# Kernel tuning notes

Hardware: AMD Instinct MI355X
Metric: run time of the kernel (lower is better)

Reference implementation:

```python
import jax, jax.numpy as jnp
import numpy as np

B, S, D = 2, 2048, 1024
H = 16
HD = D // H


def setup_inputs() -> dict:
    key = jax.random.key(0)
    k1, k2, k3 = jax.random.split(key, 3)
    x = jax.random.normal(k1, (B, S, D), dtype=jnp.float32)
    # nn.Linear(d, 3d, bias=False): weight [3d, d]; y = x @ W.T
    w_qkv = jax.random.normal(k2, (3 * D, D), dtype=jnp.float32) * (D ** -0.5)
    w_out = jax.random.normal(k3, (D, D), dtype=jnp.float32) * (D ** -0.5)
    return {"x": x, "w_qkv": w_qkv, "w_out": w_out}


def reference(x, w_qkv, w_out):
    batch, seq_len, _ = x.shape
    qkv = jnp.einsum('bsd,ed->bse', x, w_qkv)  # [B,S,3D]
    q, k, v = jnp.split(qkv, 3, axis=-1)
    # [B,S,D] -> [B,H,S,HD]
    def heads(t):
        return t.reshape(batch, seq_len, H, HD).transpose(0, 2, 1, 3)
    q, k, v = heads(q), heads(k), heads(v)
    scale = HD ** -0.5
    attn = jnp.einsum('bhqd,bhkd->bhqk', q, k) * scale  # [B,H,S,S]
    causal = jnp.triu(jnp.ones((seq_len, seq_len), dtype=bool), k=1)
    attn = jnp.where(causal, -jnp.inf, attn)
    attn = jax.nn.softmax(attn, axis=-1)
    out = jnp.einsum('bhqk,bhkd->bhqd', attn, v)  # [B,H,S,HD]
    out = out.transpose(0, 2, 1, 3).reshape(batch, seq_len, D)
    return jnp.einsum('bsd,ed->bse', out, w_out)
```

## Files before the change

kernel.cpp:

```cpp
#include <hip/hip_runtime.h>

#define NUM_B 2
#define SEQ   2048
#define DIM   1024
#define NH    16
#define HD    64

typedef __attribute__((ext_vector_type(8))) short short8;
typedef __attribute__((ext_vector_type(4))) float floatx4;
typedef unsigned short us;

#define QSCALE  0.18033688011112042f
#define SHIFT2  17.312340490667560f

#if __has_builtin(__builtin_amdgcn_exp2f)
#define EXP2(x) __builtin_amdgcn_exp2f(x)
#else
#define EXP2(x) exp2f(x)
#endif

__device__ __forceinline__ us f2bf(float f) {
    unsigned u = __float_as_uint(f);
    u += 0x7fffu + ((u >> 16) & 1u);
    return (us)(u >> 16);
}
__device__ __forceinline__ us f2bf_t(float f) {
    return (us)(__float_as_uint(f) >> 16);
}

#define GLD16(gptr, lptr) __builtin_amdgcn_global_load_lds( \
    (__attribute__((address_space(1))) unsigned int*)(gptr), \
    (__attribute__((address_space(3))) unsigned int*)(lptr), 16, 0, 0)

__global__ __launch_bounds__(256) void cast_all(
    const float* __restrict__ x, const float* __restrict__ wq,
    const float* __restrict__ wo, us* __restrict__ xb,
    us* __restrict__ wqb, us* __restrict__ wob)
{
    int i = blockIdx.x * 256 + threadIdx.x;
    const float* src; us* dst; int off;
    if (i < 524288)      { src = x;  dst = xb;  off = i; }
    else if (i < 917504) { src = wq; dst = wqb; off = i - 524288; }
    else                 { src = wo; dst = wob; off = i - 917504; }
    const float4* p = (const float4*)src + (size_t)off * 2;
    float4 f0 = p[0];
    float4 f1 = p[1];
    short8 v;
    v[0] = (short)f2bf(f0.x); v[1] = (short)f2bf(f0.y);
    v[2] = (short)f2bf(f0.z); v[3] = (short)f2bf(f0.w);
    v[4] = (short)f2bf(f1.x); v[5] = (short)f2bf(f1.y);
    v[6] = (short)f2bf(f1.z); v[7] = (short)f2bf(f1.w);
    *(short8*)(dst + (size_t)off * 8) = v;
}

__global__ __launch_bounds__(256, 2) void gemm_qkv(
    const us* __restrict__ A, const us* __restrict__ Bw,
    us* __restrict__ qb, us* __restrict__ kb, us* __restrict__ vt)
{
    __shared__ us As[128 * 64];
    __shared__ us Bs[128 * 64];
    const int t = threadIdx.x;
    const int lane = t & 63, w = t >> 6;
    const int l16 = lane & 15, quad = lane >> 4;
    const int wr = (w >> 1) * 64, wc = (w & 1) * 64;
    const int m0 = blockIdx.y * 128, n0 = blockIdx.x * 128;
    const bool isV = (blockIdx.x >= 16);
    const int srow = lane >> 3;
    const int soff = ((lane & 7) ^ srow) << 3;
    const int rsw  = l16 & 7;

    floatx4 acc[4][4];
    #pragma unroll
    for (int i = 0; i < 4; ++i)
        #pragma unroll
        for (int j = 0; j < 4; ++j) acc[i][j] = (floatx4){0.f, 0.f, 0.f, 0.f};

    for (int k0 = 0; k0 < DIM; k0 += 64) {
        #pragma unroll
        for (int c = 0; c < 4; ++c) {
            int chunk = w * 4 + c;
            int row = chunk * 8 + srow;
            GLD16(A  + (size_t)(m0 + row) * DIM + k0 + soff, &As[chunk * 512]);
            GLD16(Bw + (size_t)(n0 + row) * DIM + k0 + soff, &Bs[chunk * 512]);
        }
        __syncthreads();
        #pragma unroll
        for (int s = 0; s < 2; ++s) {
            short8 af[4], bf[4];
            #pragma unroll
            for (int i = 0; i < 4; ++i)
                af[i] = *(const short8*)&As[(wr + i * 16 + l16) * 64 + (((s * 4 + quad) ^ rsw) << 3)];
            #pragma unroll
            for (int j = 0; j < 4; ++j)
                bf[j] = *(const short8*)&Bs[(wc + j * 16 + l16) * 64 + (((s * 4 + quad) ^ rsw) << 3)];
            if (!isV) {
                #pragma unroll
                for (int i = 0; i < 4; ++i)
                    #pragma unroll
                    for (int j = 0; j < 4; ++j)
                        acc[i][j] = __builtin_amdgcn_mfma_f32_16x16x32_bf16(af[i], bf[j], acc[i][j], 0, 0, 0);
            } else {
                #pragma unroll
                for (int i = 0; i < 4; ++i)
                    #pragma unroll
                    for (int j = 0; j < 4; ++j)
                        acc[i][j] = __builtin_amdgcn_mfma_f32_16x16x32_bf16(bf[j], af[i], acc[i][j], 0, 0, 0);
            }
        }
        __syncthreads();
    }

    if (!isV) {
        const int which = n0 >> 10;
        const float sc = (which == 0) ? QSCALE : 1.0f;
        us* dst = (which == 0) ? qb : kb;
        #pragma unroll
        for (int i = 0; i < 4; ++i) {
            #pragma unroll
            for (int j = 0; j < 4; ++j) {
                int e = n0 + wc + j * 16 + l16;
                int h  = (e >> 6) & 15;
                int hd = e & 63;
                #pragma unroll
                for (int r = 0; r < 4; ++r) {
                    int m = m0 + wr + i * 16 + quad * 4 + r;
                    int b = m >> 11, s = m & 2047;
                    dst[((size_t)((b * NH + h) * SEQ + s) << 6) + hd] = f2bf(acc[i][j][r] * sc);
                }
            }
        }
    } else {
        #pragma unroll
        for (int i = 0; i < 4; ++i) {
            int m = m0 + wr + i * 16 + l16;
            int b = m >> 11, s = m & 2047;
            #pragma unroll
            for (int j = 0; j < 4; ++j) {
                int e0 = (n0 - 2048) + wc + j * 16 + quad * 4;
                #pragma unroll
                for (int r = 0; r < 4; ++r) {
                    int e = e0 + r;
                    int h = e >> 6, hd = e & 63;
                    vt[((size_t)((b * NH + h) * HD + hd) << 11) + s] = f2bf(acc[i][j][r]);
                }
            }
        }
    }
}

__global__ __launch_bounds__(256, 2) void gemm_out(
    const us* __restrict__ A, const us* __restrict__ Bw, float* __restrict__ outp)
{
    __shared__ us As[64 * 64];
    __shared__ us Bs[128 * 64];
    const int t = threadIdx.x;
    const int lane = t & 63, w = t >> 6;
    const int l16 = lane & 15, quad = lane >> 4;
    const int wr = (w >> 1) * 32, wc = (w & 1) * 64;
    const int m0 = blockIdx.y * 64, n0 = blockIdx.x * 128;
    const int srow = lane >> 3;
    const int soff = ((lane & 7) ^ srow) << 3;
    const int rsw  = l16 & 7;

    floatx4 acc[2][4];
    #pragma unroll
    for (int i = 0; i < 2; ++i)
        #pragma unroll
        for (int j = 0; j < 4; ++j) acc[i][j] = (floatx4){0.f, 0.f, 0.f, 0.f};

    for (int k0 = 0; k0 < DIM; k0 += 64) {
        #pragma unroll
        for (int c = 0; c < 2; ++c) {
            int chunk = w * 2 + c;
            int row = chunk * 8 + srow;
            GLD16(A + (size_t)(m0 + row) * DIM + k0 + soff, &As[chunk * 512]);
        }
        #pragma unroll
        for (int c = 0; c < 4; ++c) {
            int chunk = w * 4 + c;
            int row = chunk * 8 + srow;
            GLD16(Bw + (size_t)(n0 + row) * DIM + k0 + soff, &Bs[chunk * 512]);
        }
        __syncthreads();
        #pragma unroll
        for (int s = 0; s < 2; ++s) {
            short8 af[2], bf[4];
            #pragma unroll
            for (int i = 0; i < 2; ++i)
                af[i] = *(const short8*)&As[(wr + i * 16 + l16) * 64 + (((s * 4 + quad) ^ rsw) << 3)];
            #pragma unroll
            for (int j = 0; j < 4; ++j)
                bf[j] = *(const short8*)&Bs[(wc + j * 16 + l16) * 64 + (((s * 4 + quad) ^ rsw) << 3)];
            #pragma unroll
            for (int i = 0; i < 2; ++i)
                #pragma unroll
                for (int j = 0; j < 4; ++j)
                    acc[i][j] = __builtin_amdgcn_mfma_f32_16x16x32_bf16(af[i], bf[j], acc[i][j], 0, 0, 0);
        }
        __syncthreads();
    }

    #pragma unroll
    for (int i = 0; i < 2; ++i)
        #pragma unroll
        for (int j = 0; j < 4; ++j) {
            int n = n0 + wc + j * 16 + l16;
            #pragma unroll
            for (int r = 0; r < 4; ++r) {
                int m = m0 + wr + i * 16 + quad * 4 + r;
                outp[(size_t)m * DIM + n] = acc[i][j][r];
            }
        }
}

__global__ __launch_bounds__(128, 3) void attn(
    const us* __restrict__ qb, const us* __restrict__ kb,
    const us* __restrict__ vt, us* __restrict__ ob)
{
    __shared__ us Ks[64 * 64];
    __shared__ us Vs[64 * 64];
    __shared__ us Ps[2 * 32 * 72];
    const int t = threadIdx.x;
    const int lane = t & 63, w = t >> 6;
    const int l16 = lane & 15, quad = lane >> 4;
    const int idx = blockIdx.x;
    const int qt = 31 - (idx >> 5);
    const int bh = idx & 31;
    const int b = bh >> 4, h = bh & 15;
    const int q0 = qt << 6;
    const int wrow = q0 + w * 32;
    const size_t base = (size_t)bh * SEQ * HD;
    const us* qbh = qb + base;
    const us* kbh = kb + base;
    const us* vth = vt + base;
    us* Pp = Ps + w * 32 * 72;
    const int srow = lane >> 3;
    const int soff = ((lane & 7) ^ srow) << 3;
    const int rsw  = l16 & 7;

    short8 qa[2][2];
    #pragma unroll
    for (int g = 0; g < 2; ++g)
        #pragma unroll
        for (int s = 0; s < 2; ++s)
            qa[g][s] = *(const short8*)(qbh + (size_t)(wrow + g * 16 + l16) * HD + s * 32 + quad * 8);

    floatx4 o[2][4];
    #pragma unroll
    for (int g = 0; g < 2; ++g)
        #pragma unroll
        for (int j = 0; j < 4; ++j) o[g][j] = (floatx4){0.f, 0.f, 0.f, 0.f};
    float lrow[2][4] = {};

    for (int kt = 0; kt <= qt; ++kt) {
        const int j0 = kt << 6;
        #pragma unroll
        for (int c = 0; c < 4; ++c) {
            int chunk = w * 4 + c;
            int row = chunk * 8 + srow;
            GLD16(kbh + (size_t)(j0 + row) * HD + soff, &Ks[chunk * 512]);
            GLD16(vth + (size_t)row * SEQ + j0 + soff, &Vs[chunk * 512]);
        }
        __syncthreads();

        floatx4 sf[2][4];
        #pragma unroll
        for (int g = 0; g < 2; ++g)
            #pragma unroll
            for (int j = 0; j < 4; ++j)
                sf[g][j] = (floatx4){-SHIFT2, -SHIFT2, -SHIFT2, -SHIFT2};
        #pragma unroll
        for (int s = 0; s < 2; ++s)
            #pragma unroll
            for (int j = 0; j < 4; ++j) {
                short8 kf = *(const short8*)&Ks[(j * 16 + l16) * 64 + (((s * 4 + quad) ^ rsw) << 3)];
                #pragma unroll
                for (int g = 0; g < 2; ++g)
                    sf[g][j] = __builtin_amdgcn_mfma_f32_16x16x32_bf16(qa[g][s], kf, sf[g][j], 0, 0, 0);
            }

        if (kt == qt) {
            #pragma unroll
            for (int g = 0; g < 2; ++g) {
                int rowb = wrow + g * 16 + quad * 4;
                #pragma unroll
                for (int j = 0; j < 4; ++j) {
                    int colg = j0 + j * 16 + l16;
                    #pragma unroll
                    for (int r = 0; r < 4; ++r)
                        if (colg > rowb + r) sf[g][j][r] = -1e30f;
                }
            }
        }

        #pragma unroll
        for (int g = 0; g < 2; ++g) {
            float p[4][4];
            #pragma unroll
            for (int j = 0; j < 4; ++j)
                #pragma unroll
                for (int r = 0; r < 4; ++r) {
                    p[j][r] = EXP2(sf[g][j][r]);
                    Pp[(g * 16 + quad * 4 + r) * 72 + j * 16 + l16] = f2bf_t(p[j][r]);
                }
            #pragma unroll
            for (int r = 0; r < 4; ++r)
                lrow[g][r] += (p[0][r] + p[1][r]) + (p[2][r] + p[3][r]);
        }

        short8 pf[2][2];
        #pragma unroll
        for (int g = 0; g < 2; ++g)
            #pragma unroll
            for (int s = 0; s < 2; ++s)
                pf[g][s] = *(const short8*)&Pp[(g * 16 + l16) * 72 + s * 32 + quad * 8];
        #pragma unroll
        for (int s = 0; s < 2; ++s)
            #pragma unroll
            for (int j = 0; j < 4; ++j) {
                short8 vf = *(const short8*)&Vs[(j * 16 + l16) * 64 + (((s * 4 + quad) ^ rsw) << 3)];
                #pragma unroll
                for (int g = 0; g < 2; ++g)
                    o[g][j] = __builtin_amdgcn_mfma_f32_16x16x32_bf16(pf[g][s], vf, o[g][j], 0, 0, 0);
            }
        __syncthreads();
    }

    #pragma unroll
    for (int g = 0; g < 2; ++g)
        #pragma unroll
        for (int r = 0; r < 4; ++r) {
            float l = lrow[g][r];
            l += __shfl_xor(l, 1);
            l += __shfl_xor(l, 2);
            l += __shfl_xor(l, 4);
            l += __shfl_xor(l, 8);
            float inv = 1.0f / l;
            int grow = wrow + g * 16 + quad * 4 + r;
            #pragma unroll
            for (int j = 0; j < 4; ++j) {
                float val = o[g][j][r] * inv;
                ob[(size_t)(b * SEQ + grow) * DIM + h * HD + j * 16 + l16] = f2bf(val);
            }
        }
}

extern "C" void kernel_launch(void* const* d_in, const int* in_sizes, int n_in,
                              void* d_out, int out_size, void* d_ws, size_t ws_size,
                              hipStream_t stream) {
    const float* x     = (const float*)d_in[0];
    const float* w_qkv = (const float*)d_in[1];
    const float* w_out = (const float*)d_in[2];
    float* out = (float*)d_out;
    us* ws = (us*)d_ws;

    const size_t M1 = (size_t)1024 * 1024;
    us* xb  = ws;
    us* wqb = xb  + 4 * M1;
    us* wob = wqb + 3 * M1;
    us* qb  = wob + 1 * M1;
    us* kb  = qb  + 4 * M1;
    us* vt  = kb  + 4 * M1;
    us* obf = vt  + 4 * M1;

    cast_all<<<4096, 256, 0, stream>>>(x, w_qkv, w_out, xb, wqb, wob);
    gemm_qkv<<<dim3(24, 32), 256, 0, stream>>>(xb, wqb, qb, kb, vt);
    attn<<<1024, 128, 0, stream>>>(qb, kb, vt, obf);
    gemm_out<<<dim3(8, 64), 256, 0, stream>>>(obf, wob, out);
}
```

Baseline: 176.3 us.

## Rewrite attention with single-wave 32x32 MFMA tiles and register-shuffled P

The attention kernel now runs one 64-lane wave per block over 32 query rows and uses 32x32x16 MFMA with a transposed S = K·Q^T. P is passed to the PV MFMA through packed bf16 cross-half lane shuffles instead of a shared-memory round trip. K/V tiles are loaded into registers and the next tile's global-to-LDS load is issued before compute, overlapping memory with math. The grid doubles to 2048 blocks. In exchange, the 32-row causal tiles waste work on the diagonal 64-key tile, and register pressure rises with launch bounds of (64,2).

```diff
diff --git a/kernel.cpp b/kernel.cpp
--- a/kernel.cpp
+++ b/kernel.cpp
@@ -8,6 +8,8 @@
 
 typedef __attribute__((ext_vector_type(8))) short short8;
 typedef __attribute__((ext_vector_type(4))) float floatx4;
+typedef __attribute__((ext_vector_type(16))) float floatx16;
+typedef __attribute__((ext_vector_type(4))) unsigned int uint4v;
 typedef unsigned short us;
 
 #define QSCALE  0.18033688011112042f
@@ -24,8 +26,8 @@
     u += 0x7fffu + ((u >> 16) & 1u);
     return (us)(u >> 16);
 }
-__device__ __forceinline__ us f2bf_t(float f) {
-    return (us)(__float_as_uint(f) >> 16);
+__device__ __forceinline__ unsigned pk2(float lo, float hi) {
+    return (__float_as_uint(lo) >> 16) | (__float_as_uint(hi) & 0xFFFF0000u);
 }
 
 #define GLD16(gptr, lptr) __builtin_amdgcn_global_load_lds( \
@@ -213,136 +215,143 @@
         }
 }
 
-__global__ __launch_bounds__(128, 3) void attn(
+__global__ __launch_bounds__(64, 2) void attn(
     const us* __restrict__ qb, const us* __restrict__ kb,
     const us* __restrict__ vt, us* __restrict__ ob)
 {
     __shared__ us Ks[64 * 64];
     __shared__ us Vs[64 * 64];
-    __shared__ us Ps[2 * 32 * 72];
-    const int t = threadIdx.x;
-    const int lane = t & 63, w = t >> 6;
-    const int l16 = lane & 15, quad = lane >> 4;
+    const int lane = threadIdx.x;
+    const int l31 = lane & 31, hi = lane >> 5;
     const int idx = blockIdx.x;
-    const int qt = 31 - (idx >> 5);
+    const int qi = 63 - (idx >> 5);
     const int bh = idx & 31;
     const int b = bh >> 4, h = bh & 15;
-    const int q0 = qt << 6;
-    const int wrow = q0 + w * 32;
+    const int q0 = qi << 5;
+    const int nk = (qi >> 1) + 1;
     const size_t base = (size_t)bh * SEQ * HD;
     const us* qbh = qb + base;
     const us* kbh = kb + base;
     const us* vth = vt + base;
-    us* Pp = Ps + w * 32 * 72;
     const int srow = lane >> 3;
     const int soff = ((lane & 7) ^ srow) << 3;
-    const int rsw  = l16 & 7;
-
-    short8 qa[2][2];
-    #pragma unroll
-    for (int g = 0; g < 2; ++g)
-        #pragma unroll
-        for (int s = 0; s < 2; ++s)
-            qa[g][s] = *(const short8*)(qbh + (size_t)(wrow + g * 16 + l16) * HD + s * 32 + quad * 8);
-
-    floatx4 o[2][4];
-    #pragma unroll
-    for (int g = 0; g < 2; ++g)
-        #pragma unroll
-        for (int j = 0; j < 4; ++j) o[g][j] = (floatx4){0.f, 0.f, 0.f, 0.f};
-    float lrow[2][4] = {};
-
-    for (int kt = 0; kt <= qt; ++kt) {
-        const int j0 = kt << 6;
+    const int x7 = l31 & 7;
+
+    short8 qa[4];
+    #pragma unroll
+    for (int s = 0; s < 4; ++s)
+        qa[s] = *(const short8*)(qbh + (size_t)(q0 + l31) * HD + s * 16 + hi * 8);
+
+    floatx16 o[2];
+    #pragma unroll
+    for (int db = 0; db < 2; ++db)
+        #pragma unroll
+        for (int e = 0; e < 16; ++e) o[db][e] = 0.f;
+    float lsum = 0.f;
+
+    #pragma unroll
+    for (int ch = 0; ch < 8; ++ch) {
+        int row = ch * 8 + srow;
+        GLD16(kbh + (size_t)row * HD + soff, &Ks[ch * 512]);
+        GLD16(vth + (size_t)row * SEQ + soff, &Vs[ch * 512]);
+    }
+
+    for (int kt = 0; kt < nk; ++kt) {
+        __syncthreads();
+
+        short8 kf[2][4], vf[2][4];
+        #pragma unroll
+        for (int kb2 = 0; kb2 < 2; ++kb2)
+            #pragma unroll
+            for (int s = 0; s < 4; ++s)
+                kf[kb2][s] = *(const short8*)&Ks[(kb2 * 32 + l31) * 64 + (((2 * s + hi) ^ x7) << 3)];
+        #pragma unroll
+        for (int db = 0; db < 2; ++db)
+            #pragma unroll
+            for (int c = 0; c < 4; ++c)
+                vf[db][c] = *(const short8*)&Vs[(db * 32 + l31) * 64 + (((2 * c + hi) ^ x7) << 3)];
+
+        __syncthreads();
+
+        if (kt + 1 < nk) {
+            const int j0n = (kt + 1) << 6;
+            #pragma unroll
+            for (int ch = 0; ch < 8; ++ch) {
+                int row = ch * 8 + srow;
+                GLD16(kbh + (size_t)(j0n + row) * HD + soff, &Ks[ch * 512]);
+                GLD16(vth + (size_t)row * SEQ + j0n + soff, &Vs[ch * 512]);
+            }
+        }
+
+        floatx16 st[2];
+        #pragma unroll
+        for (int kb2 = 0; kb2 < 2; ++kb2)
+            #pragma unroll
+            for (int e = 0; e < 16; ++e) st[kb2][e] = -SHIFT2;
+        #pragma unroll
+        for (int kb2 = 0; kb2 < 2; ++kb2)
+            #pragma unroll
+            for (int s = 0; s < 4; ++s)
+                st[kb2] = __builtin_amdgcn_mfma_f32_32x32x16_bf16(kf[kb2][s], qa[s], st[kb2], 0, 0, 0);
+
+        if (kt == nk - 1) {
+            const int j0 = kt << 6;
+            const int myrow = q0 + l31;
+            #pragma unroll
+            for (int kb2 = 0; kb2 < 2; ++kb2)
+                #pragma unroll
+                for (int r = 0; r < 16; ++r) {
+                    int key = j0 + kb2 * 32 + (r & 3) + ((r >> 2) << 3) + (hi << 2);
+                    if (key > myrow) st[kb2][r] = -1e30f;
+                }
+        }
+
+        float pv[2][16];
+        #pragma unroll
+        for (int kb2 = 0; kb2 < 2; ++kb2)
+            #pragma unroll
+            for (int r = 0; r < 16; ++r) {
+                pv[kb2][r] = EXP2(st[kb2][r]);
+                lsum += pv[kb2][r];
+            }
+
         #pragma unroll
         for (int c = 0; c < 4; ++c) {
-            int chunk = w * 4 + c;
-            int row = chunk * 8 + srow;
-            GLD16(kbh + (size_t)(j0 + row) * HD + soff, &Ks[chunk * 512]);
-            GLD16(vth + (size_t)row * SEQ + j0 + soff, &Vs[chunk * 512]);
-        }
-        __syncthreads();
-
-        floatx4 sf[2][4];
-        #pragma unroll
-        for (int g = 0; g < 2; ++g)
-            #pragma unroll
-            for (int j = 0; j < 4; ++j)
-                sf[g][j] = (floatx4){-SHIFT2, -SHIFT2, -SHIFT2, -SHIFT2};
-        #pragma unroll
-        for (int s = 0; s < 2; ++s)
-            #pragma unroll
-            for (int j = 0; j < 4; ++j) {
-                short8 kf = *(const short8*)&Ks[(j * 16 + l16) * 64 + (((s * 4 + quad) ^ rsw) << 3)];
-                #pragma unroll
-                for (int g = 0; g < 2; ++g)
-                    sf[g][j] = __builtin_amdgcn_mfma_f32_16x16x32_bf16(qa[g][s], kf, sf[g][j], 0, 0, 0);
-            }
-
-        if (kt == qt) {
-            #pragma unroll
-            for (int g = 0; g < 2; ++g) {
-                int rowb = wrow + g * 16 + quad * 4;
-                #pragma unroll
-                for (int j = 0; j < 4; ++j) {
-                    int colg = j0 + j * 16 + l16;
-                    #pragma unroll
-                    for (int r = 0; r < 4; ++r)
-                        if (colg > rowb + r) sf[g][j][r] = -1e30f;
-                }
-            }
-        }
-
-        #pragma unroll
-        for (int g = 0; g < 2; ++g) {
-            float p[4][4];
-            #pragma unroll
-            for (int j = 0; j < 4; ++j)
-                #pragma unroll
-                for (int r = 0; r < 4; ++r) {
-                    p[j][r] = EXP2(sf[g][j][r]);
-                    Pp[(g * 16 + quad * 4 + r) * 72 + j * 16 + l16] = f2bf_t(p[j][r]);
-                }
-            #pragma unroll
-            for (int r = 0; r < 4; ++r)
-                lrow[g][r] += (p[0][r] + p[1][r]) + (p[2][r] + p[3][r]);
-        }
-
-        short8 pf[2][2];
-        #pragma unroll
-        for (int g = 0; g < 2; ++g)
-            #pragma unroll
-            for (int s = 0; s < 2; ++s)
-                pf[g][s] = *(const short8*)&Pp[(g * 16 + l16) * 72 + s * 32 + quad * 8];
-        #pragma unroll
-        for (int s = 0; s < 2; ++s)
-            #pragma unroll
-            for (int j = 0; j < 4; ++j) {
-                short8 vf = *(const short8*)&Vs[(j * 16 + l16) * 64 + (((s * 4 + quad) ^ rsw) << 3)];
-                #pragma unroll
-                for (int g = 0; g < 2; ++g)
-                    o[g][j] = __builtin_amdgcn_mfma_f32_16x16x32_bf16(pf[g][s], vf, o[g][j], 0, 0, 0);
-            }
-        __syncthreads();
-    }
-
-    #pragma unroll
-    for (int g = 0; g < 2; ++g)
-        #pragma unroll
-        for (int r = 0; r < 4; ++r) {
-            float l = lrow[g][r];
-            l += __shfl_xor(l, 1);
-            l += __shfl_xor(l, 2);
-            l += __shfl_xor(l, 4);
-            l += __shfl_xor(l, 8);
-            float inv = 1.0f / l;
-            int grow = wrow + g * 16 + quad * 4 + r;
-            #pragma unroll
-            for (int j = 0; j < 4; ++j) {
-                float val = o[g][j][r] * inv;
-                ob[(size_t)(b * SEQ + grow) * DIM + h * HD + j * 16 + l16] = f2bf(val);
-            }
-        }
+            const int kb2 = c >> 1;
+            const int rb = (c & 1) * 8;
+            unsigned a0 = pk2(pv[kb2][rb + 0], pv[kb2][rb + 1]);
+            unsigned a1 = pk2(pv[kb2][rb + 2], pv[kb2][rb + 3]);
+            unsigned b0 = pk2(pv[kb2][rb + 4], pv[kb2][rb + 5]);
+            unsigned b1 = pk2(pv[kb2][rb + 6], pv[kb2][rb + 7]);
+            unsigned s0 = hi ? a0 : b0;
+            unsigned s1 = hi ? a1 : b1;
+            unsigned r0 = __shfl_xor((int)s0, 32);
+            unsigned r1 = __shfl_xor((int)s1, 32);
+            uint4v fd;
+            fd[0] = hi ? r0 : a0;
+            fd[1] = hi ? r1 : a1;
+            fd[2] = hi ? b0 : r0;
+            fd[3] = hi ? b1 : r1;
+            short8 pf = *(short8*)&fd;
+            #pragma unroll
+            for (int db = 0; db < 2; ++db)
+                o[db] = __builtin_amdgcn_mfma_f32_32x32x16_bf16(pf, vf[db][c], o[db], 0, 0, 0);
+        }
+    }
+
+    lsum += __shfl_xor(lsum, 32);
+    float linv = 1.0f / lsum;
+    #pragma unroll
+    for (int r = 0; r < 16; ++r) {
+        int row = (r & 3) + ((r >> 2) << 3) + (hi << 2);
+        float lr = __shfl(linv, row);
+        int grow = q0 + row;
+        #pragma unroll
+        for (int db = 0; db < 2; ++db) {
+            int d = db * 32 + l31;
+            ob[(size_t)(b * SEQ + grow) * DIM + h * HD + d] = f2bf(o[db][r] * lr);
+        }
+    }
 }
 
 extern "C" void kernel_launch(void* const* d_in, const int* in_sizes, int n_in,
@@ -365,6 +374,6 @@
 
     cast_all<<<4096, 256, 0, stream>>>(x, w_qkv, w_out, xb, wqb, wob);
     gemm_qkv<<<dim3(24, 32), 256, 0, stream>>>(xb, wqb, qb, kb, vt);
-    attn<<<1024, 128, 0, stream>>>(qb, kb, vt, obf);
+    attn<<<2048, 64, 0, stream>>>(qb, kb, vt, obf);
     gemm_out<<<dim3(8, 64), 256, 0, stream>>>(obf, wob, out);
 }
```

New measurement: 174.0 us. No clear change (-1.3%).
